# Kernel tuning notes

Hardware: AMD Instinct MI355X
Metric: run time of the kernel (lower is better)

The kernel has to match this reference:

```python
import jax, jax.numpy as jnp
import numpy as np

B, D, H, W_, C = 2, 64, 64, 64, 96
EPS = 1e-5


def _merge(t):
    # t: [b, d, h, w, c] -> [b, d/2, h/2, w/2, 8*c], channel blocks ordered
    # by itertools.product(i, j, k): block index = i*4 + j*2 + k.
    b, d, h, w, c = t.shape
    t = t.reshape(b, d // 2, 2, h // 2, 2, w // 2, 2, c)
    t = t.transpose(0, 1, 3, 5, 2, 4, 6, 7)  # i slowest, then j, then k
    return t.reshape(b, d // 2, h // 2, w // 2, 8 * c)


def setup_inputs() -> dict:
    key = jax.random.key(0)
    k1, k2, k3 = jax.random.split(key, 3)
    x = jax.random.normal(k1, (B, D, H, W_, C), dtype=jnp.float32)
    mask = jax.random.bernoulli(k2, 0.7, (B, D, H, W_, 1)).astype(jnp.float32)
    gamma = jnp.ones((8 * C,), dtype=jnp.float32)
    beta = jnp.zeros((8 * C,), dtype=jnp.float32)
    W = (jax.random.normal(k3, (8 * C, 2 * C), dtype=jnp.float32)
         / np.float32(np.sqrt(8 * C)))  # Linear(8*dim, 2*dim, bias=False), stored [in, out]
    return {"x": x, "mask": mask, "gamma": gamma, "beta": beta, "W": W}


def reference(x, mask, gamma, beta, W):
    xm = x * mask  # broadcast of [b,d,h,w,1] mask over channels
    xr = _merge(xm)            # [b, d/2, h/2, w/2, 8c]
    mr = _merge(mask)          # [b, d/2, h/2, w/2, 8]
    mask_out = mr.sum(axis=-1) > 0
    # LayerNorm over last (8c) dim, biased variance, eps=1e-5
    mu = xr.mean(axis=-1, keepdims=True)
    var = jnp.mean(jnp.square(xr - mu), axis=-1, keepdims=True)
    xn = (xr - mu) * jax.lax.rsqrt(var + EPS) * gamma + beta
    out = jnp.einsum('bdhwc,co->bdhwo', xn, W)  # [b, d/2, h/2, w/2, 2*dim]
    return out, mask_out
```

## Files before the change

### kernel.cpp

```cpp
#include <hip/hip_runtime.h>

#define C8   768
#define NOUT 192
#define M_TOTAL 65536
#define OUT0 (M_TOTAL * NOUT)

typedef __attribute__((ext_vector_type(8))) short  short8;
typedef __attribute__((ext_vector_type(4))) float  f32x4;
typedef __attribute__((ext_vector_type(4))) unsigned short us4;

__device__ __forceinline__ unsigned short f2bf(float f) {
    union { float f; unsigned u; } a; a.f = f;
    unsigned r = a.u + 0x7FFFu + ((a.u >> 16) & 1u);
    return (unsigned short)(r >> 16);
}

__global__ __launch_bounds__(256) void prepw_kernel(const float* __restrict__ Wm,
                                                    unsigned short* __restrict__ Wb) {
    int t = blockIdx.x * 256 + threadIdx.x;
    if (t >= 24 * 12 * 512) return;
    int e  = t & 7;
    int l  = (t >> 3) & 63;
    int f  = t >> 9;
    int fn = f % 12;
    int ks = f / 12;
    int k = ks * 32 + ((l >> 4) << 3) + e;
    int n = fn * 16 + (l & 15);
    Wb[t] = f2bf(Wm[k * NOUT + n]);
}

__global__ __launch_bounds__(256) void fused_kernel(
    const float* __restrict__ x, const float* __restrict__ mask,
    const float* __restrict__ gamma, const float* __restrict__ beta,
    const unsigned short* __restrict__ Wb, float* __restrict__ out)
{
    __shared__ unsigned short Alds[32 * 768];
    const int tid = threadIdx.x;
    const int l   = tid & 63;
    const int wv  = tid >> 6;
    const int rowbase = blockIdx.x * 32;

    for (int i = 0; i < 8; ++i) {
        const int r  = (wv << 3) + i;
        const int rg = rowbase + r;
        const int w2 = rg & 31, h2 = (rg >> 5) & 31, d2 = (rg >> 10) & 31, b = rg >> 15;
        const int vbase = ((b * 64 + d2 * 2) * 64 + h2 * 2) * 64 + w2 * 2;

        float vs[12];
        float s = 0.f, s2 = 0.f;
#pragma unroll
        for (int m = 0; m < 3; ++m) {
            const int c8 = (m << 8) + (l << 2);
            const int bi = c8 / 96;
            const int ch = c8 - bi * 96;
            const int voff = vbase + ((bi >> 2) * 64 + ((bi >> 1) & 1)) * 64 + (bi & 1);
            const float4 v = *(const float4*)(x + (size_t)voff * 96 + ch);
            const float mv = mask[voff];
            const float a0 = v.x * mv, a1 = v.y * mv, a2 = v.z * mv, a3 = v.w * mv;
            vs[m * 4 + 0] = a0; vs[m * 4 + 1] = a1; vs[m * 4 + 2] = a2; vs[m * 4 + 3] = a3;
            s  += (a0 + a1) + (a2 + a3);
            s2 += (a0 * a0 + a1 * a1) + (a2 * a2 + a3 * a3);
        }
#pragma unroll
        for (int off = 32; off >= 1; off >>= 1) {
            s  += __shfl_xor(s,  off);
            s2 += __shfl_xor(s2, off);
        }
        const float mu  = s * (1.f / 768.f);
        const float var = s2 * (1.f / 768.f) - mu * mu;
        const float rs  = rsqrtf(var + 1e-5f);
        const int swz = (r & 7) << 4;
        char* rowp = (char*)Alds + r * 1536;
#pragma unroll
        for (int m = 0; m < 3; ++m) {
            const int c8 = (m << 8) + (l << 2);
            const float4 g  = *(const float4*)(gamma + c8);
            const float4 bt = *(const float4*)(beta  + c8);
            us4 o;
            o.x = f2bf((vs[m * 4 + 0] - mu) * rs * g.x + bt.x);
            o.y = f2bf((vs[m * 4 + 1] - mu) * rs * g.y + bt.y);
            o.z = f2bf((vs[m * 4 + 2] - mu) * rs * g.z + bt.z);
            o.w = f2bf((vs[m * 4 + 3] - mu) * rs * g.w + bt.w);
            *(us4*)(rowp + ((c8 << 1) ^ swz)) = o;
        }
        if (l == 0) {
            float ms = 0.f;
#pragma unroll
            for (int bi = 0; bi < 8; ++bi)
                ms += mask[vbase + ((bi >> 2) * 64 + ((bi >> 1) & 1)) * 64 + (bi & 1)];
            out[OUT0 + rg] = (ms > 0.f) ? 1.0f : 0.0f;
        }
    }
    __syncthreads();

    f32x4 acc[2][3] = {};
    const int lrow = l & 15;
    const int kq   = (l >> 4) << 4;
    const int swz2 = (l & 7) << 4;
    const char* aBase = (const char*)Alds + lrow * 1536;
    const short8* Wv = (const short8*)Wb;
    const int bbase = wv * 3 * 64 + l;

#pragma unroll 2
    for (int ks = 0; ks < 24; ++ks) {
        const int ko = ((ks << 6) + kq) ^ swz2;
        short8 a0 = *(const short8*)(aBase + ko);
        short8 a1 = *(const short8*)(aBase + 16 * 1536 + ko);
        short8 b0 = Wv[ks * 768 + bbase];
        short8 b1 = Wv[ks * 768 + bbase + 64];
        short8 b2 = Wv[ks * 768 + bbase + 128];
        acc[0][0] = __builtin_amdgcn_mfma_f32_16x16x32_bf16(a0, b0, acc[0][0], 0, 0, 0);
        acc[1][0] = __builtin_amdgcn_mfma_f32_16x16x32_bf16(a1, b0, acc[1][0], 0, 0, 0);
        acc[0][1] = __builtin_amdgcn_mfma_f32_16x16x32_bf16(a0, b1, acc[0][1], 0, 0, 0);
        acc[1][1] = __builtin_amdgcn_mfma_f32_16x16x32_bf16(a1, b1, acc[1][1], 0, 0, 0);
        acc[0][2] = __builtin_amdgcn_mfma_f32_16x16x32_bf16(a0, b2, acc[0][2], 0, 0, 0);
        acc[1][2] = __builtin_amdgcn_mfma_f32_16x16x32_bf16(a1, b2, acc[1][2], 0, 0, 0);
    }

    const int colb = wv * 48 + lrow;
    const int r0   = rowbase + ((l >> 4) << 2);
#pragma unroll
    for (int fm = 0; fm < 2; ++fm)
#pragma unroll
        for (int fn = 0; fn < 3; ++fn)
#pragma unroll
            for (int j = 0; j < 4; ++j)
                out[(size_t)(r0 + fm * 16 + j) * NOUT + colb + fn * 16] = acc[fm][fn][j];
}

extern "C" void kernel_launch(void* const* d_in, const int* in_sizes, int n_in,
                              void* d_out, int out_size, void* d_ws, size_t ws_size,
                              hipStream_t stream) {
    const float* x     = (const float*)d_in[0];
    const float* mask  = (const float*)d_in[1];
    const float* gamma = (const float*)d_in[2];
    const float* beta  = (const float*)d_in[3];
    const float* Wm    = (const float*)d_in[4];
    float* out = (float*)d_out;
    unsigned short* Wb = (unsigned short*)d_ws;

    prepw_kernel<<<576, 256, 0, stream>>>(Wm, Wb);
    fused_kernel<<<2048, 256, 0, stream>>>(x, mask, gamma, beta, Wb, out);
}
```

Baseline: 78.32 us.

## Split K across 8 waves per block and reduce partial sums through LDS

Each block now runs 512 threads (8 waves). The LayerNorm rows are spread across all 8 waves, and the GEMM K dimension is split between two halves of 4 waves each. The two sets of partial accumulators are summed through LDS, which also stages the output tile so it can be written back as coalesced float4 stores instead of scattered scalar stores. The aim is more waves in flight to hide memory latency and better-coalesced output writes. The cost is extra barriers, LDS traffic for the reduction, and tighter register limits from launch_bounds(512,6).

```diff
diff --git a/kernel.cpp b/kernel.cpp
--- a/kernel.cpp
+++ b/kernel.cpp
@@ -4,6 +4,7 @@
 #define NOUT 192
 #define M_TOTAL 65536
 #define OUT0 (M_TOTAL * NOUT)
+#define CLDS_STRIDE 196
 
 typedef __attribute__((ext_vector_type(8))) short  short8;
 typedef __attribute__((ext_vector_type(4))) float  f32x4;
@@ -29,19 +30,23 @@
     Wb[t] = f2bf(Wm[k * NOUT + n]);
 }
 
-__global__ __launch_bounds__(256) void fused_kernel(
+__global__ __launch_bounds__(512, 6) void fused_kernel(
     const float* __restrict__ x, const float* __restrict__ mask,
     const float* __restrict__ gamma, const float* __restrict__ beta,
     const unsigned short* __restrict__ Wb, float* __restrict__ out)
 {
-    __shared__ unsigned short Alds[32 * 768];
+    __shared__ __align__(16) char smem[49152];
+    unsigned short* Alds = (unsigned short*)smem;
+    float*          Clds = (float*)smem;
+
     const int tid = threadIdx.x;
     const int l   = tid & 63;
     const int wv  = tid >> 6;
     const int rowbase = blockIdx.x * 32;
 
-    for (int i = 0; i < 8; ++i) {
-        const int r  = (wv << 3) + i;
+#pragma unroll 2
+    for (int i = 0; i < 4; ++i) {
+        const int r  = (wv << 2) + i;
         const int rg = rowbase + r;
         const int w2 = rg & 31, h2 = (rg >> 5) & 31, d2 = (rg >> 10) & 31, b = rg >> 15;
         const int vbase = ((b * 64 + d2 * 2) * 64 + h2 * 2) * 64 + w2 * 2;
@@ -93,16 +98,18 @@
     }
     __syncthreads();
 
+    const int cg = wv & 3;
+    const int kh = wv >> 2;
     f32x4 acc[2][3] = {};
     const int lrow = l & 15;
     const int kq   = (l >> 4) << 4;
     const int swz2 = (l & 7) << 4;
     const char* aBase = (const char*)Alds + lrow * 1536;
     const short8* Wv = (const short8*)Wb;
-    const int bbase = wv * 3 * 64 + l;
+    const int bbase = cg * 192 + l;
 
 #pragma unroll 2
-    for (int ks = 0; ks < 24; ++ks) {
+    for (int ks = kh * 12; ks < kh * 12 + 12; ++ks) {
         const int ko = ((ks << 6) + kq) ^ swz2;
         short8 a0 = *(const short8*)(aBase + ko);
         short8 a1 = *(const short8*)(aBase + 16 * 1536 + ko);
@@ -117,15 +124,39 @@
         acc[1][2] = __builtin_amdgcn_mfma_f32_16x16x32_bf16(a1, b2, acc[1][2], 0, 0, 0);
     }
 
-    const int colb = wv * 48 + lrow;
-    const int r0   = rowbase + ((l >> 4) << 2);
+    __syncthreads();
+    if (kh == 1) {
 #pragma unroll
-    for (int fm = 0; fm < 2; ++fm)
+        for (int fm = 0; fm < 2; ++fm)
 #pragma unroll
-        for (int fn = 0; fn < 3; ++fn)
+            for (int fn = 0; fn < 3; ++fn)
 #pragma unroll
-            for (int j = 0; j < 4; ++j)
-                out[(size_t)(r0 + fm * 16 + j) * NOUT + colb + fn * 16] = acc[fm][fn][j];
+                for (int j = 0; j < 4; ++j) {
+                    const int row = fm * 16 + ((l >> 4) << 2) + j;
+                    const int col = cg * 48 + fn * 16 + lrow;
+                    Clds[row * CLDS_STRIDE + col] = acc[fm][fn][j];
+                }
+    }
+    __syncthreads();
+    if (kh == 0) {
+#pragma unroll
+        for (int fm = 0; fm < 2; ++fm)
+#pragma unroll
+            for (int fn = 0; fn < 3; ++fn)
+#pragma unroll
+                for (int j = 0; j < 4; ++j) {
+                    const int row = fm * 16 + ((l >> 4) << 2) + j;
+                    const int col = cg * 48 + fn * 16 + lrow;
+                    Clds[row * CLDS_STRIDE + col] += acc[fm][fn][j];
+                }
+    }
+    __syncthreads();
+#pragma unroll
+    for (int idx = tid; idx < 32 * 48; idx += 512) {
+        const int row = idx / 48, c4 = idx % 48;
+        const float4 v = *(const float4*)&Clds[row * CLDS_STRIDE + c4 * 4];
+        *(float4*)&out[(size_t)(rowbase + row) * NOUT + c4 * 4] = v;
+    }
 }
 
 extern "C" void kernel_launch(void* const* d_in, const int* in_sizes, int n_in,
@@ -140,5 +171,5 @@
     unsigned short* Wb = (unsigned short*)d_ws;
 
     prepw_kernel<<<576, 256, 0, stream>>>(Wm, Wb);
-    fused_kernel<<<2048, 256, 0, stream>>>(x, mask, gamma, beta, Wb, out);
+    fused_kernel<<<2048, 512, 0, stream>>>(x, mask, gamma, beta, Wb, out);
 }
```

Result: slower. 87.49 us (+11.7%).

## Stage x via async global-to-LDS loads, halve row tile, stage output through LDS

Applied to the files above, without the earlier changes.

The kernel now fetches the raw x rows straight into LDS with global_load_lds, so the loads are issued asynchronously up front instead of per row in a serial loop. The mask is gathered once into LDS and the mask output comes from there. Rows per block drop from 32 to 16 and the grid doubles, with a launch-bounds occupancy hint of 3. Results are staged through padded LDS so the output store uses coalesced float4 writes. In exchange, each block reuses every W fragment over half as many rows (one A fragment instead of two), so W traffic per output row doubles, and more barriers are added.

```diff
diff --git a/kernel.cpp b/kernel.cpp
--- a/kernel.cpp
+++ b/kernel.cpp
@@ -1,9 +1,9 @@
 #include <hip/hip_runtime.h>
 
-#define C8   768
 #define NOUT 192
 #define M_TOTAL 65536
 #define OUT0 (M_TOTAL * NOUT)
+#define CSTRIDE 196
 
 typedef __attribute__((ext_vector_type(8))) short  short8;
 typedef __attribute__((ext_vector_type(4))) float  f32x4;
@@ -15,6 +15,11 @@
     return (unsigned short)(r >> 16);
 }
 
+__device__ __forceinline__ void gload16(void* lds, const void* g) {
+    __builtin_amdgcn_global_load_lds((const __attribute__((address_space(1))) void*)g,
+                                     (__attribute__((address_space(3))) void*)lds, 16, 0, 0);
+}
+
 __global__ __launch_bounds__(256) void prepw_kernel(const float* __restrict__ Wm,
                                                     unsigned short* __restrict__ Wb) {
     int t = blockIdx.x * 256 + threadIdx.x;
@@ -24,108 +29,153 @@
     int f  = t >> 9;
     int fn = f % 12;
     int ks = f / 12;
-    int k = ks * 32 + ((l >> 4) << 3) + e;
-    int n = fn * 16 + (l & 15);
-    Wb[t] = f2bf(Wm[k * NOUT + n]);
+    Wb[t] = f2bf(Wm[(ks * 32 + ((l >> 4) << 3) + e) * NOUT + fn * 16 + (l & 15)]);
 }
 
-__global__ __launch_bounds__(256) void fused_kernel(
+__global__ __launch_bounds__(256, 3) void fused_kernel(
     const float* __restrict__ x, const float* __restrict__ mask,
     const float* __restrict__ gamma, const float* __restrict__ beta,
     const unsigned short* __restrict__ Wb, float* __restrict__ out)
 {
-    __shared__ unsigned short Alds[32 * 768];
+    __shared__ __align__(16) float rawf[16 * 768];
+    __shared__ __align__(16) float maskLds[16 * 8];
+
     const int tid = threadIdx.x;
     const int l   = tid & 63;
     const int wv  = tid >> 6;
-    const int rowbase = blockIdx.x * 32;
+    const int rowbase = blockIdx.x * 16;
 
-    for (int i = 0; i < 8; ++i) {
-        const int r  = (wv << 3) + i;
+    int bi_[3], ch_[3], vo_[3];
+#pragma unroll
+    for (int m = 0; m < 3; ++m) {
+        const int c8 = (m << 8) + (l << 2);
+        const int bi = c8 / 96;
+        bi_[m] = bi;
+        ch_[m] = c8 - bi * 96;
+        vo_[m] = ((bi >> 2) << 12) + (((bi >> 1) & 1) << 6) + (bi & 1);
+    }
+
+#pragma unroll
+    for (int rr = 0; rr < 4; ++rr) {
+        const int r  = (wv << 2) + rr;
         const int rg = rowbase + r;
         const int w2 = rg & 31, h2 = (rg >> 5) & 31, d2 = (rg >> 10) & 31, b = rg >> 15;
         const int vbase = ((b * 64 + d2 * 2) * 64 + h2 * 2) * 64 + w2 * 2;
+#pragma unroll
+        for (int m = 0; m < 3; ++m)
+            gload16(&rawf[r * 768 + (m << 8)],
+                    x + (size_t)(vbase + vo_[m]) * 96 + ch_[m]);
+    }
 
-        float vs[12];
-        float s = 0.f, s2 = 0.f;
+    if (tid < 128) {
+        const int r = tid >> 3, bi = tid & 7;
+        const int rg = rowbase + r;
+        const int w2 = rg & 31, h2 = (rg >> 5) & 31, d2 = (rg >> 10) & 31, b = rg >> 15;
+        const int vbase = ((b * 64 + d2 * 2) * 64 + h2 * 2) * 64 + w2 * 2;
+        maskLds[tid] = mask[vbase + ((bi >> 2) << 12) + (((bi >> 1) & 1) << 6) + (bi & 1)];
+    }
+
+    float4 g_[3], be_[3];
+#pragma unroll
+    for (int m = 0; m < 3; ++m) {
+        const int c8 = (m << 8) + (l << 2);
+        g_[m]  = *(const float4*)(gamma + c8);
+        be_[m] = *(const float4*)(beta  + c8);
+    }
+
+    __syncthreads();
+
+    if (tid < 16) {
+        float ms = 0.f;
+#pragma unroll
+        for (int i = 0; i < 8; ++i) ms += maskLds[tid * 8 + i];
+        out[OUT0 + rowbase + tid] = (ms > 0.f) ? 1.0f : 0.0f;
+    }
+
+    float4 vs[4][3];
+    float  s[4], s2[4];
+#pragma unroll
+    for (int rr = 0; rr < 4; ++rr) {
+        const int r = (wv << 2) + rr;
 #pragma unroll
         for (int m = 0; m < 3; ++m) {
-            const int c8 = (m << 8) + (l << 2);
-            const int bi = c8 / 96;
-            const int ch = c8 - bi * 96;
-            const int voff = vbase + ((bi >> 2) * 64 + ((bi >> 1) & 1)) * 64 + (bi & 1);
-            const float4 v = *(const float4*)(x + (size_t)voff * 96 + ch);
-            const float mv = mask[voff];
-            const float a0 = v.x * mv, a1 = v.y * mv, a2 = v.z * mv, a3 = v.w * mv;
-            vs[m * 4 + 0] = a0; vs[m * 4 + 1] = a1; vs[m * 4 + 2] = a2; vs[m * 4 + 3] = a3;
-            s  += (a0 + a1) + (a2 + a3);
-            s2 += (a0 * a0 + a1 * a1) + (a2 * a2 + a3 * a3);
+            float4 v = *(const float4*)&rawf[r * 768 + (m << 8) + (l << 2)];
+            const float mk = maskLds[r * 8 + bi_[m]];
+            v.x *= mk; v.y *= mk; v.z *= mk; v.w *= mk;
+            vs[rr][m] = v;
         }
-#pragma unroll
-        for (int off = 32; off >= 1; off >>= 1) {
-            s  += __shfl_xor(s,  off);
-            s2 += __shfl_xor(s2, off);
-        }
-        const float mu  = s * (1.f / 768.f);
-        const float var = s2 * (1.f / 768.f) - mu * mu;
-        const float rs  = rsqrtf(var + 1e-5f);
-        const int swz = (r & 7) << 4;
-        char* rowp = (char*)Alds + r * 1536;
+        float a = 0.f, b2 = 0.f;
 #pragma unroll
         for (int m = 0; m < 3; ++m) {
-            const int c8 = (m << 8) + (l << 2);
-            const float4 g  = *(const float4*)(gamma + c8);
-            const float4 bt = *(const float4*)(beta  + c8);
+            const float4 v = vs[rr][m];
+            a  += (v.x + v.y) + (v.z + v.w);
+            b2 += (v.x * v.x + v.y * v.y) + (v.z * v.z + v.w * v.w);
+        }
+        s[rr] = a; s2[rr] = b2;
+    }
+#pragma unroll
+    for (int off = 32; off >= 1; off >>= 1) {
+#pragma unroll
+        for (int rr = 0; rr < 4; ++rr) {
+            s[rr]  += __shfl_xor(s[rr],  off);
+            s2[rr] += __shfl_xor(s2[rr], off);
+        }
+    }
+#pragma unroll
+    for (int rr = 0; rr < 4; ++rr) {
+        const int r = (wv << 2) + rr;
+        const float mu  = s[rr] * (1.f / 768.f);
+        const float var = s2[rr] * (1.f / 768.f) - mu * mu;
+        const float rs  = rsqrtf(var + 1e-5f);
+        char* abase = (char*)rawf + r * 3072;
+        const int swz = (r & 7) << 4;
+#pragma unroll
+        for (int m = 0; m < 3; ++m) {
+            const float4 v = vs[rr][m];
             us4 o;
-            o.x = f2bf((vs[m * 4 + 0] - mu) * rs * g.x + bt.x);
-            o.y = f2bf((vs[m * 4 + 1] - mu) * rs * g.y + bt.y);
-            o.z = f2bf((vs[m * 4 + 2] - mu) * rs * g.z + bt.z);
-            o.w = f2bf((vs[m * 4 + 3] - mu) * rs * g.w + bt.w);
-            *(us4*)(rowp + ((c8 << 1) ^ swz)) = o;
-        }
-        if (l == 0) {
-            float ms = 0.f;
-#pragma unroll
-            for (int bi = 0; bi < 8; ++bi)
-                ms += mask[vbase + ((bi >> 2) * 64 + ((bi >> 1) & 1)) * 64 + (bi & 1)];
-            out[OUT0 + rg] = (ms > 0.f) ? 1.0f : 0.0f;
+            o.x = f2bf((v.x - mu) * rs * g_[m].x + be_[m].x);
+            o.y = f2bf((v.y - mu) * rs * g_[m].y + be_[m].y);
+            o.z = f2bf((v.z - mu) * rs * g_[m].z + be_[m].z);
+            o.w = f2bf((v.w - mu) * rs * g_[m].w + be_[m].w);
+            *(us4*)(abase + (((m << 9) + (l << 3)) ^ swz)) = o;
         }
     }
     __syncthreads();
 
-    f32x4 acc[2][3] = {};
+    f32x4 acc[3] = {};
     const int lrow = l & 15;
     const int kq   = (l >> 4) << 4;
-    const int swz2 = (l & 7) << 4;
-    const char* aBase = (const char*)Alds + lrow * 1536;
+    const int aswz = (lrow & 7) << 4;
+    const char* aBase = (const char*)rawf + lrow * 3072;
     const short8* Wv = (const short8*)Wb;
-    const int bbase = wv * 3 * 64 + l;
+    const int bbase = wv * 192 + l;
 
-#pragma unroll 2
+#pragma unroll 4
     for (int ks = 0; ks < 24; ++ks) {
-        const int ko = ((ks << 6) + kq) ^ swz2;
-        short8 a0 = *(const short8*)(aBase + ko);
-        short8 a1 = *(const short8*)(aBase + 16 * 1536 + ko);
-        short8 b0 = Wv[ks * 768 + bbase];
-        short8 b1 = Wv[ks * 768 + bbase + 64];
-        short8 b2 = Wv[ks * 768 + bbase + 128];
-        acc[0][0] = __builtin_amdgcn_mfma_f32_16x16x32_bf16(a0, b0, acc[0][0], 0, 0, 0);
-        acc[1][0] = __builtin_amdgcn_mfma_f32_16x16x32_bf16(a1, b0, acc[1][0], 0, 0, 0);
-        acc[0][1] = __builtin_amdgcn_mfma_f32_16x16x32_bf16(a0, b1, acc[0][1], 0, 0, 0);
-        acc[1][1] = __builtin_amdgcn_mfma_f32_16x16x32_bf16(a1, b1, acc[1][1], 0, 0, 0);
-        acc[0][2] = __builtin_amdgcn_mfma_f32_16x16x32_bf16(a0, b2, acc[0][2], 0, 0, 0);
-        acc[1][2] = __builtin_amdgcn_mfma_f32_16x16x32_bf16(a1, b2, acc[1][2], 0, 0, 0);
+        const short8 a  = *(const short8*)(aBase + ((((ks << 6) + kq)) ^ aswz));
+        const short8 b0 = Wv[ks * 768 + bbase];
+        const short8 b1 = Wv[ks * 768 + bbase + 64];
+        const short8 b2 = Wv[ks * 768 + bbase + 128];
+        acc[0] = __builtin_amdgcn_mfma_f32_16x16x32_bf16(a, b0, acc[0], 0, 0, 0);
+        acc[1] = __builtin_amdgcn_mfma_f32_16x16x32_bf16(a, b1, acc[1], 0, 0, 0);
+        acc[2] = __builtin_amdgcn_mfma_f32_16x16x32_bf16(a, b2, acc[2], 0, 0, 0);
     }
 
-    const int colb = wv * 48 + lrow;
-    const int r0   = rowbase + ((l >> 4) << 2);
+    __syncthreads();
+    float* Clds = rawf;
 #pragma unroll
-    for (int fm = 0; fm < 2; ++fm)
+    for (int c = 0; c < 3; ++c)
 #pragma unroll
-        for (int fn = 0; fn < 3; ++fn)
+        for (int j = 0; j < 4; ++j)
+            Clds[(((l >> 4) << 2) + j) * CSTRIDE + wv * 48 + c * 16 + lrow] = acc[c][j];
+    __syncthreads();
+
 #pragma unroll
-            for (int j = 0; j < 4; ++j)
-                out[(size_t)(r0 + fm * 16 + j) * NOUT + colb + fn * 16] = acc[fm][fn][j];
+    for (int idx = tid; idx < 16 * 48; idx += 256) {
+        const int row = idx / 48, c4 = idx % 48;
+        *(float4*)&out[(size_t)(rowbase + row) * NOUT + (c4 << 2)] =
+            *(const float4*)&Clds[row * CSTRIDE + (c4 << 2)];
+    }
 }
 
 extern "C" void kernel_launch(void* const* d_in, const int* in_sizes, int n_in,
@@ -140,5 +190,5 @@
     unsigned short* Wb = (unsigned short*)d_ws;
 
     prepw_kernel<<<576, 256, 0, stream>>>(Wm, Wb);
-    fused_kernel<<<2048, 256, 0, stream>>>(x, mask, gamma, beta, Wb, out);
+    fused_kernel<<<4096, 256, 0, stream>>>(x, mask, gamma, beta, Wb, out);
 }
```

Result: slower. 92.75 us (+18.4%).
